# Performance work log

Hardware: AMD Instinct MI355X
Metric: run time of the kernel (lower is better)

The kernel has to match this reference:

```python
import jax, jax.numpy as jnp
import numpy as np

C = 512          # resnet18 feature_dim
HID = 256        # relation_hidden_dim
B, Hh, Ww = 8, 14, 14


def setup_inputs() -> dict:
    key = jax.random.key(0)
    k1, k2, k3, k4, k5 = jax.random.split(key, 5)
    f1 = jax.random.normal(k1, (B, C, Hh, Ww), dtype=jnp.float32)
    f2 = jax.random.normal(k2, (B, C, Hh, Ww), dtype=jnp.float32)
    # relation head params (Linear(2C -> HID), ReLU, Linear(HID -> 1))
    s1 = 1.0 / np.sqrt(2 * C)
    s2 = 1.0 / np.sqrt(HID)
    W1 = jax.random.uniform(k3, (2 * C, HID), jnp.float32, -s1, s1)
    b1 = jnp.zeros((HID,), jnp.float32)
    W2 = jax.random.uniform(k4, (HID, 1), jnp.float32, -s2, s2)
    b2 = jnp.zeros((1,), jnp.float32)
    return {"f1": f1, "f2": f2, "W1": W1, "b1": b1, "W2": W2, "b2": b2}


def reference(f1, f2, W1, b1, W2, b2):
    # f1, f2: [B, C, h, w] encoder feature maps
    b, c, h, w = f1.shape
    L = h * w
    # [B, L, C]
    x1 = f1.reshape(b, c, L).transpose(0, 2, 1)
    x2 = f2.reshape(b, c, L).transpose(0, 2, 1)
    # Algebraic split of first Linear over the concat:
    # cat([f1_i, f2_j]) @ W1 == f1_i @ W1[:C] + f2_j @ W1[C:]
    p1 = jnp.einsum('blc,ch->blh', x1, W1[:c])      # [B, L, HID]
    p2 = jnp.einsum('blc,ch->blh', x2, W1[c:])      # [B, L, HID]
    hid = jax.nn.relu(p1[:, :, None, :] + p2[:, None, :, :] + b1)  # [B, L, L, HID]
    scores = jnp.einsum('bijh,ho->bijo', hid, W2) + b2  # [B, L, L, 1]
    sim = scores.reshape(b, L * L).sum(axis=1, keepdims=True)  # aggregation='sum'
    return sim
```

## Files before the change

### kernel.cpp

```cpp
#include <hip/hip_runtime.h>

typedef __attribute__((ext_vector_type(8))) short bf16x8;
typedef __attribute__((ext_vector_type(4))) float f32x4;

#define C_DIM 512
#define HID   256
#define B_DIM 8
#define L_DIM 196
#define MTPB  7
#define NT    32
#define NNT   (HID/NT)
#define GEMM_BLOCKS (B_DIM*MTPB*NNT*2)
#define ROWS  14
#define NJC   14
#define JCL   (L_DIM/NJC)
#define PAIR_BLOCKS ((B_DIM*NJC*ROWS)/4)
#define P_ELEMS (B_DIM*L_DIM*HID)

__device__ __forceinline__ short bf16r(float x) {
  unsigned u = __builtin_bit_cast(unsigned, x);
  return (short)((u + 0x8000u) >> 16);
}

__global__ __launch_bounds__(256) void gemm_p_mfma(
    const float* __restrict__ f1, const float* __restrict__ f2,
    const float* __restrict__ W1, const float* __restrict__ b1,
    const float* __restrict__ b2,
    float* __restrict__ p1, float* __restrict__ p2,
    float* __restrict__ out) {
  if (blockIdx.x == 0 && threadIdx.x < B_DIM)
    out[threadIdx.x] = (float)(L_DIM * L_DIM) * b2[0];

  const int wgid = blockIdx.x;
  const int b    = wgid & 7;
  const int idx  = wgid >> 3;
  const int nt   = idx & 7;
  const int ms   = idx >> 3;
  const int side = ms & 1;
  const int mt   = ms >> 1;

  const float* __restrict__ f = side ? f2 : f1;
  const float* __restrict__ W = W1 + side * C_DIM * HID;
  float* __restrict__ p = side ? p2 : p1;

  const int tid  = threadIdx.x;
  const int kq   = tid >> 6;
  const int lane = tid & 63;
  const int g    = lane >> 4;
  const int mcol = lane & 15;

  int aoff[2];
  #pragma unroll
  for (int mi = 0; mi < 2; ++mi) {
    const int rib = mt * 32 + mi * 16 + mcol;
    const int l = rib < L_DIM ? rib : L_DIM - 1;
    aoff[mi] = (b * C_DIM) * L_DIM + l;
  }
  const int h0 = nt * NT + mcol;

  f32x4 acc[2][2];
  #pragma unroll
  for (int mi = 0; mi < 2; ++mi)
    #pragma unroll
    for (int ni = 0; ni < 2; ++ni)
      acc[mi][ni] = (f32x4){0.f, 0.f, 0.f, 0.f};

  #pragma unroll
  for (int ks = 0; ks < 4; ++ks) {
    const int k0 = kq * 128 + ks * 32 + g * 8;
    bf16x8 afr[2], bfr[2];
    #pragma unroll
    for (int mi = 0; mi < 2; ++mi) {
      const float* __restrict__ pa = f + aoff[mi] + k0 * L_DIM;
      #pragma unroll
      for (int i = 0; i < 8; ++i) afr[mi][i] = bf16r(pa[i * L_DIM]);
    }
    #pragma unroll
    for (int ni = 0; ni < 2; ++ni) {
      const float* __restrict__ pb = W + k0 * HID + h0 + ni * 16;
      #pragma unroll
      for (int i = 0; i < 8; ++i) bfr[ni][i] = bf16r(pb[i * HID]);
    }
    #pragma unroll
    for (int mi = 0; mi < 2; ++mi)
      #pragma unroll
      for (int ni = 0; ni < 2; ++ni)
        acc[mi][ni] = __builtin_amdgcn_mfma_f32_16x16x32_bf16(
            afr[mi], bfr[ni], acc[mi][ni], 0, 0, 0);
  }

  __shared__ float comb[2][64][17];
  if (kq >= 2) {
    #pragma unroll
    for (int mi = 0; mi < 2; ++mi)
      #pragma unroll
      for (int ni = 0; ni < 2; ++ni)
        *(float4*)&comb[kq - 2][lane][mi * 8 + ni * 4] =
            *(float4*)&acc[mi][ni];
  }
  __syncthreads();
  if (kq < 2) {
    #pragma unroll
    for (int mi = 0; mi < 2; ++mi)
      #pragma unroll
      for (int ni = 0; ni < 2; ++ni) {
        const float4 o = *(const float4*)&comb[kq][lane][mi * 8 + ni * 4];
        acc[mi][ni][0] += o.x; acc[mi][ni][1] += o.y;
        acc[mi][ni][2] += o.z; acc[mi][ni][3] += o.w;
      }
  }
  __syncthreads();
  if (kq == 1) {
    #pragma unroll
    for (int mi = 0; mi < 2; ++mi)
      #pragma unroll
      for (int ni = 0; ni < 2; ++ni)
        *(float4*)&comb[0][lane][mi * 8 + ni * 4] = *(float4*)&acc[mi][ni];
  }
  __syncthreads();
  if (kq == 0) {
    #pragma unroll
    for (int mi = 0; mi < 2; ++mi) {
      const int rib0 = mt * 32 + mi * 16 + g * 4;
      #pragma unroll
      for (int ni = 0; ni < 2; ++ni) {
        const int h = h0 + ni * 16;
        const float bias = side ? 0.0f : b1[h];
        const float4 o = *(const float4*)&comb[0][lane][mi * 8 + ni * 4];
        const float v0 = acc[mi][ni][0] + o.x + bias;
        const float v1 = acc[mi][ni][1] + o.y + bias;
        const float v2 = acc[mi][ni][2] + o.z + bias;
        const float v3 = acc[mi][ni][3] + o.w + bias;
        if (rib0 + 0 < L_DIM) p[(b * L_DIM + rib0 + 0) * HID + h] = v0;
        if (rib0 + 1 < L_DIM) p[(b * L_DIM + rib0 + 1) * HID + h] = v1;
        if (rib0 + 2 < L_DIM) p[(b * L_DIM + rib0 + 2) * HID + h] = v2;
        if (rib0 + 3 < L_DIM) p[(b * L_DIM + rib0 + 3) * HID + h] = v3;
      }
    }
  }
}

__global__ __launch_bounds__(256, 1) void pair_kernel(
    const float* __restrict__ p1, const float* __restrict__ p2,
    const float* __restrict__ W2, float* __restrict__ out) {
  const int lane = threadIdx.x & 63;
  const int w    = threadIdx.x >> 6;
  const int b    = blockIdx.x & 7;
  const int idx  = blockIdx.x >> 3;
  const int r4   = idx * 4 + w;
  const int jc   = r4 / ROWS;
  const int wi   = r4 % ROWS;

  const float4 wv = *(const float4*)(W2 + lane * 4);
  const float* __restrict__ p1b = p1 + (b * L_DIM) * HID + lane * 4;

  float4 a[ROWS];
  #pragma unroll
  for (int k = 0; k < ROWS; ++k)
    a[k] = *(const float4*)(p1b + (wi + k * ROWS) * HID);

  float s[ROWS];
  #pragma unroll
  for (int k = 0; k < ROWS; ++k) s[k] = 0.0f;

  const float4* __restrict__ vp =
      (const float4*)(p2 + (b * L_DIM + jc * JCL) * HID) + lane;

#define PAIR_BODY(vv)                                            \
  {                                                              \
    _Pragma("unroll")                                            \
    for (int k = 0; k < ROWS; ++k) {                             \
      s[k] = fmaf(fmaxf(a[k].x + (vv).x, 0.f), wv.x, s[k]);      \
      s[k] = fmaf(fmaxf(a[k].y + (vv).y, 0.f), wv.y, s[k]);      \
      s[k] = fmaf(fmaxf(a[k].z + (vv).z, 0.f), wv.z, s[k]);      \
      s[k] = fmaf(fmaxf(a[k].w + (vv).w, 0.f), wv.w, s[k]);      \
    }                                                            \
  }

  float4 vv[7];
  #pragma unroll
  for (int j = 0; j < 7; ++j) vv[j] = vp[j * (HID / 4)];
  #pragma unroll
  for (int j = 0; j < 7; ++j) PAIR_BODY(vv[j]);
  #pragma unroll
  for (int j = 0; j < 7; ++j) vv[j] = vp[(7 + j) * (HID / 4)];
  #pragma unroll
  for (int j = 0; j < 7; ++j) PAIR_BODY(vv[j]);
#undef PAIR_BODY

  float t = 0.0f;
  #pragma unroll
  for (int k = 0; k < ROWS; ++k) t += s[k];
  #pragma unroll
  for (int off = 32; off > 0; off >>= 1) t += __shfl_down(t, off);

  __shared__ float sred[4];
  if (lane == 0) sred[w] = t;
  __syncthreads();
  if (threadIdx.x == 0)
    atomicAdd(&out[b], sred[0] + sred[1] + sred[2] + sred[3]);
}

extern "C" void kernel_launch(void* const* d_in, const int* in_sizes, int n_in,
                              void* d_out, int out_size, void* d_ws, size_t ws_size,
                              hipStream_t stream) {
  const float* f1 = (const float*)d_in[0];
  const float* f2 = (const float*)d_in[1];
  const float* W1 = (const float*)d_in[2];
  const float* b1 = (const float*)d_in[3];
  const float* W2 = (const float*)d_in[4];
  const float* b2 = (const float*)d_in[5];
  float* out = (float*)d_out;

  float* p1 = (float*)d_ws;
  float* p2 = p1 + P_ELEMS;

  gemm_p_mfma<<<GEMM_BLOCKS, 256, 0, stream>>>(f1, f2, W1, b1, b2, p1, p2, out);

  pair_kernel<<<PAIR_BLOCKS, 256, 0, stream>>>(p1, p2, W2, out);
}
```

Before: 27.20 us.

## Fuse projection GEMM and pair kernel with per-batch spin barrier

Merges the MFMA projection GEMM and the pairwise ReLU-reduction kernel into one launch. Blocks sync per batch through an atomic counter and spin-wait before the pair phase. The GEMM tile is widened from 32 to 64 hidden columns, halving the block count to 448 so all blocks can be co-resident. This removes one kernel launch and the gap between kernels, but adds a memset launch and relies on every block being resident at once; otherwise the spin barrier deadlocks.

```diff
diff --git a/kernel.cpp b/kernel.cpp
--- a/kernel.cpp
+++ b/kernel.cpp
@@ -7,48 +7,40 @@
 #define HID   256
 #define B_DIM 8
 #define L_DIM 196
-#define MTPB  7
-#define NT    32
-#define NNT   (HID/NT)
-#define GEMM_BLOCKS (B_DIM*MTPB*NNT*2)
 #define ROWS  14
 #define NJC   14
-#define JCL   (L_DIM/NJC)
-#define PAIR_BLOCKS ((B_DIM*NJC*ROWS)/4)
+#define JCL   14
 #define P_ELEMS (B_DIM*L_DIM*HID)
+#define BLOCKS_PER_B 56
+#define FUSED_BLOCKS (B_DIM*BLOCKS_PER_B)
 
 __device__ __forceinline__ short bf16r(float x) {
   unsigned u = __builtin_bit_cast(unsigned, x);
   return (short)((u + 0x8000u) >> 16);
 }
 
-__global__ __launch_bounds__(256) void gemm_p_mfma(
+__global__ __launch_bounds__(256, 2) void fused_kernel(
     const float* __restrict__ f1, const float* __restrict__ f2,
     const float* __restrict__ W1, const float* __restrict__ b1,
-    const float* __restrict__ b2,
+    const float* __restrict__ b2, const float* __restrict__ W2,
     float* __restrict__ p1, float* __restrict__ p2,
-    float* __restrict__ out) {
-  if (blockIdx.x == 0 && threadIdx.x < B_DIM)
-    out[threadIdx.x] = (float)(L_DIM * L_DIM) * b2[0];
-
-  const int wgid = blockIdx.x;
-  const int b    = wgid & 7;
-  const int idx  = wgid >> 3;
-  const int nt   = idx & 7;
-  const int ms   = idx >> 3;
-  const int side = ms & 1;
-  const int mt   = ms >> 1;
-
-  const float* __restrict__ f = side ? f2 : f1;
-  const float* __restrict__ W = W1 + side * C_DIM * HID;
-  float* __restrict__ p = side ? p2 : p1;
-
+    int* __restrict__ sem, float* __restrict__ out) {
+  const int b    = blockIdx.x & 7;
+  const int idx  = blockIdx.x >> 3;
   const int tid  = threadIdx.x;
   const int kq   = tid >> 6;
   const int lane = tid & 63;
   const int g    = lane >> 4;
   const int mcol = lane & 15;
 
+  const int ms   = idx >> 2;
+  const int ntp  = idx & 3;
+  const int side = ms & 1;
+  const int mt   = ms >> 1;
+  const float* __restrict__ f = side ? f2 : f1;
+  const float* __restrict__ W = W1 + side * C_DIM * HID;
+  float* __restrict__ p = side ? p2 : p1;
+
   int aoff[2];
   #pragma unroll
   for (int mi = 0; mi < 2; ++mi) {
@@ -56,19 +48,19 @@
     const int l = rib < L_DIM ? rib : L_DIM - 1;
     aoff[mi] = (b * C_DIM) * L_DIM + l;
   }
-  const int h0 = nt * NT + mcol;
-
-  f32x4 acc[2][2];
+  const int h0 = ntp * 64 + mcol;
+
+  f32x4 acc[2][4];
   #pragma unroll
   for (int mi = 0; mi < 2; ++mi)
     #pragma unroll
-    for (int ni = 0; ni < 2; ++ni)
+    for (int ni = 0; ni < 4; ++ni)
       acc[mi][ni] = (f32x4){0.f, 0.f, 0.f, 0.f};
 
   #pragma unroll
   for (int ks = 0; ks < 4; ++ks) {
     const int k0 = kq * 128 + ks * 32 + g * 8;
-    bf16x8 afr[2], bfr[2];
+    bf16x8 afr[2], bfr[4];
     #pragma unroll
     for (int mi = 0; mi < 2; ++mi) {
       const float* __restrict__ pa = f + aoff[mi] + k0 * L_DIM;
@@ -76,7 +68,7 @@
       for (int i = 0; i < 8; ++i) afr[mi][i] = bf16r(pa[i * L_DIM]);
     }
     #pragma unroll
-    for (int ni = 0; ni < 2; ++ni) {
+    for (int ni = 0; ni < 4; ++ni) {
       const float* __restrict__ pb = W + k0 * HID + h0 + ni * 16;
       #pragma unroll
       for (int i = 0; i < 8; ++i) bfr[ni][i] = bf16r(pb[i * HID]);
@@ -84,27 +76,26 @@
     #pragma unroll
     for (int mi = 0; mi < 2; ++mi)
       #pragma unroll
-      for (int ni = 0; ni < 2; ++ni)
+      for (int ni = 0; ni < 4; ++ni)
         acc[mi][ni] = __builtin_amdgcn_mfma_f32_16x16x32_bf16(
             afr[mi], bfr[ni], acc[mi][ni], 0, 0, 0);
   }
 
-  __shared__ float comb[2][64][17];
+  __shared__ float comb[2][64][33];
   if (kq >= 2) {
     #pragma unroll
     for (int mi = 0; mi < 2; ++mi)
       #pragma unroll
-      for (int ni = 0; ni < 2; ++ni)
-        *(float4*)&comb[kq - 2][lane][mi * 8 + ni * 4] =
-            *(float4*)&acc[mi][ni];
+      for (int ni = 0; ni < 4; ++ni)
+        *(float4*)&comb[kq - 2][lane][mi * 16 + ni * 4] = *(float4*)&acc[mi][ni];
   }
   __syncthreads();
   if (kq < 2) {
     #pragma unroll
     for (int mi = 0; mi < 2; ++mi)
       #pragma unroll
-      for (int ni = 0; ni < 2; ++ni) {
-        const float4 o = *(const float4*)&comb[kq][lane][mi * 8 + ni * 4];
+      for (int ni = 0; ni < 4; ++ni) {
+        const float4 o = *(const float4*)&comb[kq][lane][mi * 16 + ni * 4];
         acc[mi][ni][0] += o.x; acc[mi][ni][1] += o.y;
         acc[mi][ni][2] += o.z; acc[mi][ni][3] += o.w;
       }
@@ -114,8 +105,8 @@
     #pragma unroll
     for (int mi = 0; mi < 2; ++mi)
       #pragma unroll
-      for (int ni = 0; ni < 2; ++ni)
-        *(float4*)&comb[0][lane][mi * 8 + ni * 4] = *(float4*)&acc[mi][ni];
+      for (int ni = 0; ni < 4; ++ni)
+        *(float4*)&comb[0][lane][mi * 16 + ni * 4] = *(float4*)&acc[mi][ni];
   }
   __syncthreads();
   if (kq == 0) {
@@ -123,10 +114,10 @@
     for (int mi = 0; mi < 2; ++mi) {
       const int rib0 = mt * 32 + mi * 16 + g * 4;
       #pragma unroll
-      for (int ni = 0; ni < 2; ++ni) {
+      for (int ni = 0; ni < 4; ++ni) {
         const int h = h0 + ni * 16;
         const float bias = side ? 0.0f : b1[h];
-        const float4 o = *(const float4*)&comb[0][lane][mi * 8 + ni * 4];
+        const float4 o = *(const float4*)&comb[0][lane][mi * 16 + ni * 4];
         const float v0 = acc[mi][ni][0] + o.x + bias;
         const float v1 = acc[mi][ni][1] + o.y + bias;
         const float v2 = acc[mi][ni][2] + o.z + bias;
@@ -138,18 +129,27 @@
       }
     }
   }
-}
-
-__global__ __launch_bounds__(256, 1) void pair_kernel(
-    const float* __restrict__ p1, const float* __restrict__ p2,
-    const float* __restrict__ W2, float* __restrict__ out) {
-  const int lane = threadIdx.x & 63;
-  const int w    = threadIdx.x >> 6;
-  const int b    = blockIdx.x & 7;
-  const int idx  = blockIdx.x >> 3;
-  const int r4   = idx * 4 + w;
-  const int jc   = r4 / ROWS;
-  const int wi   = r4 % ROWS;
+
+  if (idx == 0 && tid == 0)
+    __hip_atomic_store(&out[b], (float)(L_DIM * L_DIM) * b2[0],
+                       __ATOMIC_RELAXED, __HIP_MEMORY_SCOPE_AGENT);
+
+  __syncthreads();
+  if (tid == 0) {
+    __builtin_amdgcn_fence(__ATOMIC_RELEASE, "agent");
+    atomicAdd(&sem[b], 1);
+    while (__hip_atomic_load(&sem[b], __ATOMIC_RELAXED,
+                             __HIP_MEMORY_SCOPE_AGENT) < BLOCKS_PER_B)
+      __builtin_amdgcn_s_sleep(2);
+    __builtin_amdgcn_fence(__ATOMIC_ACQUIRE, "agent");
+  }
+  __syncthreads();
+
+  if (idx >= 49) return;
+
+  const int r4 = idx * 4 + kq;
+  const int jc = r4 / ROWS;
+  const int wi = r4 % ROWS;
 
   const float4 wv = *(const float4*)(W2 + lane * 4);
   const float* __restrict__ p1b = p1 + (b * L_DIM) * HID + lane * 4;
@@ -195,9 +195,9 @@
   for (int off = 32; off > 0; off >>= 1) t += __shfl_down(t, off);
 
   __shared__ float sred[4];
-  if (lane == 0) sred[w] = t;
-  __syncthreads();
-  if (threadIdx.x == 0)
+  if (lane == 0) sred[kq] = t;
+  __syncthreads();
+  if (tid == 0)
     atomicAdd(&out[b], sred[0] + sred[1] + sred[2] + sred[3]);
 }
 
@@ -214,8 +214,10 @@
 
   float* p1 = (float*)d_ws;
   float* p2 = p1 + P_ELEMS;
-
-  gemm_p_mfma<<<GEMM_BLOCKS, 256, 0, stream>>>(f1, f2, W1, b1, b2, p1, p2, out);
-
-  pair_kernel<<<PAIR_BLOCKS, 256, 0, stream>>>(p1, p2, W2, out);
+  int* sem  = (int*)(p2 + P_ELEMS);
+
+  hipMemsetAsync(sem, 0, B_DIM * sizeof(int), stream);
+
+  fused_kernel<<<FUSED_BLOCKS, 256, 0, stream>>>(
+      f1, f2, W1, b1, b2, W2, p1, p2, sem, out);
 }
```

After: 62.70 us. 2.31x slower.
